# Performance work log

Measured on AMD Instinct MI355X. Metric: run time of the kernel, lower is better.

Reference implementation:

```python
import jax, jax.numpy as jnp
import numpy as np

B, T, W = 64, 64, 20
VIDEO_DIM = 1024
JOINT_DIM = 1024
K, STRIDE = 4, 4
MARGIN = 0.2
EPS = 1e-8


def _l2norm(x, axis=-1):
    n = jnp.sqrt(jnp.sum(x * x, axis=axis, keepdims=True))
    return x / jnp.maximum(n, EPS)


def _conv1d(x, w, b, stride):
    # x: (B, C, L), w: (O, I, K) -> (B, O, L_out), VALID padding (padding=0)
    y = jax.lax.conv_general_dilated(x, w, (stride,), 'VALID',
                                     dimension_numbers=('NCH', 'OIH', 'NCH'))
    return y + b[None, :, None]


def _diag_loss(scores, margin):
    # faithful port of diag(): row/column margin costs with zeroed diagonal
    b = scores.shape[0]
    d = jnp.diagonal(scores)
    off = 1.0 - jnp.eye(b, dtype=scores.dtype)
    cost_s = jnp.maximum(margin + scores - d[:, None], 0.0) * off
    cost_im = jnp.maximum(margin + scores - d[None, :], 0.0) * off
    return cost_s.sum() / b + cost_im.sum() / b


def setup_inputs() -> dict:
    key = jax.random.key(0)
    ks = jax.random.split(key, 10)
    def g(k, shape, scale=0.02):
        return jax.random.normal(k, shape, dtype=jnp.float32) * scale
    return dict(
        video=jax.random.normal(ks[0], (B, T, VIDEO_DIM), dtype=jnp.float32),
        words=jax.random.normal(ks[1], (B, W, JOINT_DIM), dtype=jnp.float32),
        w_masks=jnp.ones((B, W), dtype=jnp.int32),
        sentences=jax.random.normal(ks[2], (B, JOINT_DIM), dtype=jnp.float32),
        conv0_w=g(ks[3], (JOINT_DIM, VIDEO_DIM, K)),
        conv0_b=jnp.zeros((JOINT_DIM,), jnp.float32),
        conv1_w=g(ks[4], (JOINT_DIM, JOINT_DIM, K)),
        conv1_b=jnp.zeros((JOINT_DIM,), jnp.float32),
        conv2_w=g(ks[5], (JOINT_DIM, JOINT_DIM, K)),
        conv2_b=jnp.zeros((JOINT_DIM,), jnp.float32),
        conv1d_w=g(ks[6], (JOINT_DIM, JOINT_DIM, 1)),
        conv1d_b=jnp.zeros((JOINT_DIM,), jnp.float32),
        fc_w=g(ks[7], (JOINT_DIM, JOINT_DIM)),
        fc_b=jnp.zeros((JOINT_DIM,), jnp.float32),
    )


def reference(video, words, w_masks, sentences,
              conv0_w, conv0_b, conv1_w, conv1_b, conv2_w, conv2_b,
              conv1d_w, conv1d_b, fc_w, fc_b):
    # Vectorizes the original per-sample python loop over the pair axes (i=sentence, j=video).
    x = jnp.transpose(video, (0, 2, 1))          # (B, C, T)
    wmask = (w_masks > 0)                        # (B, W)
    conv_params = [(conv0_w, conv0_b), (conv1_w, conv1_b), (conv2_w, conv2_b)]
    sims = []
    v_tmp = x
    for cw, cb in conv_params:
        v_tmp = jax.nn.relu(_conv1d(v_tmp, cw, cb, STRIDE))
        v = jnp.transpose(_conv1d(v_tmp, conv1d_w, conv1d_b, 1), (0, 2, 1))  # (B, Tl, D)
        # frame_by_word: masked softmax attention of frames over words
        att = jnp.einsum('jtd,iwd->ijtw', v, words)            # (i, j, Tl, W)
        att = jnp.where(wmask[:, None, None, :], att, -1e30)
        att = jax.nn.softmax(att, axis=-1)
        v_s = jnp.einsum('ijtw,iwd->ijtd', att, words)         # attended word ctx
        # cosine sim of l2-normed vectors == dot product
        sim = jnp.einsum('jtd,ijtd->ijt', _l2norm(v), _l2norm(v_s))
        sims.append(sim)
    score_all = jnp.concatenate(sims, axis=2)    # (B, B, T_total=21)
    # torch code sorts descending then means over dim 1 -> mean is sort-invariant
    scores = score_all.mean(axis=2)              # (B, B) local scores
    positive_map = score_all[jnp.arange(B), jnp.arange(B)]     # (B, T_total)
    # global branch: final conv output has length 1 -> squeeze
    g_v = _l2norm(v_tmp[:, :, 0] @ fc_w.T + fc_b)              # (B, D), unit norm
    g_scores = _l2norm(sentences) @ g_v.T                      # [i, j] = cos(g_v[j], sent[i])
    loss = _diag_loss(scores, MARGIN) + _diag_loss(g_scores, MARGIN)
    return loss, positive_map
```

## Files before the change

kernel.cpp:

```cpp
#include <hip/hip_runtime.h>
#include <cmath>
#include <cstdint>


typedef __bf16 bf16_t;
typedef bf16_t bf16x8 __attribute__((ext_vector_type(8)));
typedef bf16_t bf16x4 __attribute__((ext_vector_type(4)));
typedef float  f32x4  __attribute__((ext_vector_type(4)));

#define CP0_SL   1048576
#define CP1_SL   262144
#define CPC0_SL  1048576
#define CP2_SL   65536
#define CPC1_SL  262144
#define CPC2_SL  65536
#define CPFC_SL  65536
#define CPAT_SL  1720320

#define MFMA16(a,b,c) __builtin_amdgcn_mfma_f32_16x16x32_bf16(a, b, c, 0, 0, 0)

__device__ __forceinline__ void gload_lds16(const void* g, void* l) {
    __builtin_amdgcn_global_load_lds(
        (const __attribute__((address_space(1))) void*)g,
        (__attribute__((address_space(3))) void*)l, 16, 0, 0);
}

__device__ __forceinline__ int swz(int r, int c) { return (r * 8 + (c ^ (r & 7))) * 8; }

__device__ __forceinline__ void gemm64(
    const bf16_t* __restrict__ A, const bf16_t* __restrict__ B,
    float* __restrict__ Cz, int Nc, int K,
    int m0A, int n0B, int k0, int nIt, int m0C, int n0C,
    bf16_t* sA, bf16_t* sB)
{
    const int tid  = threadIdx.x;
    const int lane = tid & 63, wave = tid >> 6;
    const int sr = tid >> 3, pc = tid & 7, lc = pc ^ (sr & 7);
    const bf16_t* Ag = A + (size_t)(m0A + sr) * K + k0 + lc * 8;
    const bf16_t* Bg = B + (size_t)(n0B + sr) * K + k0 + lc * 8;
    const size_t rowskip = (size_t)32 * K;
    const int wr = (wave >> 1) * 32, wc = (wave & 1) * 32;
    const int fm = lane & 15, cb = lane >> 4;
    int offA[2][2], offB[2][2];
    #pragma unroll
    for (int h = 0; h < 2; h++) {
        offA[h][0] = swz(wr +      fm, cb + h * 4);
        offA[h][1] = swz(wr + 16 + fm, cb + h * 4);
        offB[h][0] = swz(wc +      fm, cb + h * 4);
        offB[h][1] = swz(wc + 16 + fm, cb + h * 4);
    }
    f32x4 acc[2][2];
    #pragma unroll
    for (int a = 0; a < 2; a++)
        #pragma unroll
        for (int b = 0; b < 2; b++) acc[a][b] = (f32x4){0.f, 0.f, 0.f, 0.f};

    gload_lds16(Ag,           sA + tid * 8);
    gload_lds16(Ag + rowskip, sA + 2048 + tid * 8);
    gload_lds16(Bg,           sB + tid * 8);
    gload_lds16(Bg + rowskip, sB + 2048 + tid * 8);
    for (int it = 0; it < nIt; ++it) {
        const int buf = it & 1;
        const bf16_t* cA = sA + buf * 4096;
        const bf16_t* cB = sB + buf * 4096;
        __syncthreads();
        if (it + 1 < nIt) {
            const bf16_t* a = Ag + (it + 1) * 64;
            const bf16_t* b = Bg + (it + 1) * 64;
            bf16_t* dA = sA + (buf ^ 1) * 4096;
            bf16_t* dB = sB + (buf ^ 1) * 4096;
            gload_lds16(a,           dA + tid * 8);
            gload_lds16(a + rowskip, dA + 2048 + tid * 8);
            gload_lds16(b,           dB + tid * 8);
            gload_lds16(b + rowskip, dB + 2048 + tid * 8);
        }
        #pragma unroll
        for (int h = 0; h < 2; h++) {
            bf16x8 a0 = *(const bf16x8*)&cA[offA[h][0]];
            bf16x8 a1 = *(const bf16x8*)&cA[offA[h][1]];
            bf16x8 b0 = *(const bf16x8*)&cB[offB[h][0]];
            bf16x8 b1 = *(const bf16x8*)&cB[offB[h][1]];
            acc[0][0] = MFMA16(a0, b0, acc[0][0]);
            acc[0][1] = MFMA16(a0, b1, acc[0][1]);
            acc[1][0] = MFMA16(a1, b0, acc[1][0]);
            acc[1][1] = MFMA16(a1, b1, acc[1][1]);
        }
    }
    #pragma unroll
    for (int im = 0; im < 2; im++)
        #pragma unroll
        for (int rr = 0; rr < 4; rr++) {
            int gm = m0C + wr + im * 16 + cb * 4 + rr;
            #pragma unroll
            for (int in_ = 0; in_ < 2; in_++) {
                int cg = n0C + wc + in_ * 16 + fm;
                Cz[(size_t)gm * Nc + cg] = acc[im][in_][rr];
            }
        }
}

__device__ __forceinline__ void rownorm_row(const bf16_t* __restrict__ VCb,
                                            float* __restrict__ VN, int r, int tid)
{
    const int lane = tid & 63;
    const bf16_t* x = VCb + ((size_t)r << 10) + lane * 16;
    bf16x8 v0 = *(const bf16x8*)x, v1 = *(const bf16x8*)(x + 8);
    float s = 0.f;
    #pragma unroll
    for (int e = 0; e < 8; e++) {
        float a = (float)v0[e], b = (float)v1[e];
        s += a * a + b * b;
    }
    #pragma unroll
    for (int o = 32; o; o >>= 1) s += __shfl_xor(s, o, 64);
    if (lane == 0) VN[r] = sqrtf(s);
}

__device__ __forceinline__ void sim_compute(
    int i, int c, const float* __restrict__ CPat, const float* __restrict__ VN,
    const float* Gs, const float* msk, float* __restrict__ SA)
{
    float s[20], p[20];
    float mx = -1e30f;
    #pragma unroll
    for (int w = 0; w < 20; w++) {
        size_t q = (size_t)(i * 20 + w) * 1344 + c;
        s[w] = CPat[q] + CPat[q + CPAT_SL];
        if (msk[w] != 0.f) mx = fmaxf(mx, s[w]);
    }
    float denom = 0.f, num = 0.f;
    #pragma unroll
    for (int w = 0; w < 20; w++) {
        p[w] = (msk[w] != 0.f) ? __expf(s[w] - mx) : 0.f;
        denom += p[w];
        num   += p[w] * s[w];
    }
    float quad = 0.f;
    #pragma unroll
    for (int w = 0; w < 20; w++) {
        float cc = 0.f;
        #pragma unroll
        for (int w2 = 0; w2 < 20; w2++) cc += Gs[w * 20 + w2] * p[w2];
        quad += p[w] * cc;
    }
    float dot = num / denom;
    float vsn = sqrtf(fmaxf(quad, 0.f)) / denom;
    float sim = dot / (fmaxf(VN[c], 1e-8f) * fmaxf(vsn, 1e-8f));
    int j, t;
    if (c < 1024)      { j = c >> 4;          t = c & 15; }
    else if (c < 1280) { j = (c - 1024) >> 2; t = 16 + ((c - 1024) & 3); }
    else               { j = c - 1280;        t = 20; }
    SA[((size_t)i * 64 + j) * 21 + t] = sim;
}

__global__ __launch_bounds__(256) void prep0_kernel(
    const float* __restrict__ c0w, bf16_t* __restrict__ WT0,
    const float* __restrict__ video, bf16_t* __restrict__ Vb)
{
    int bx = blockIdx.x;
    if (bx < 4096) {
        int idx = bx * 256 + threadIdx.x;
        int i = idx & 1023, o = idx >> 10;
        float4 v = *(const float4*)(c0w + ((size_t)o << 12) + (i << 2));
        bf16_t* base = WT0 + ((size_t)o << 12) + i;
        base[0]    = (bf16_t)v.x;
        base[1024] = (bf16_t)v.y;
        base[2048] = (bf16_t)v.z;
        base[3072] = (bf16_t)v.w;
    } else {
        int off = ((bx - 4096) * 256 + threadIdx.x) * 4;
        float4 v = *(const float4*)(video + off);
        bf16x4 o4 = { (bf16_t)v.x, (bf16_t)v.y, (bf16_t)v.z, (bf16_t)v.w };
        *(bf16x4*)(Vb + off) = o4;
    }
}

__global__ __launch_bounds__(256) void d2_kernel(
    const bf16_t* __restrict__ Vb, const bf16_t* __restrict__ WT0, float* __restrict__ CP0,
    const float* __restrict__ c1w, const float* __restrict__ c2w,
    bf16_t* __restrict__ WT1, bf16_t* __restrict__ WT2,
    const float* __restrict__ words, bf16_t* __restrict__ Wordsb,
    const float* __restrict__ c1dw, bf16_t* __restrict__ C1b,
    const float* __restrict__ fcw, bf16_t* __restrict__ Fb)
{
    __shared__ __align__(16) bf16_t sA[2][8192];
    __shared__ __align__(16) bf16_t sB[2][8192];
    const int bx = blockIdx.x, tid = threadIdx.x;
    if (bx < 512) {
        const int z = bx >> 6, rem = bx & 63, xt = rem & 7, yt = rem >> 3;
        const int m0 = xt * 128, n0 = yt * 128, k0 = z * 512;
        const int lane = tid & 63, wave = tid >> 6;
        const int sr = tid >> 3, pc = tid & 7, lc = pc ^ (sr & 7);
        const bf16_t* Ag = Vb  + (size_t)(m0 + sr) * 4096 + k0 + lc * 8;
        const bf16_t* Bg = WT0 + (size_t)(n0 + sr) * 4096 + k0 + lc * 8;
        const size_t rowskip = (size_t)32 * 4096;
        const int wrow = (wave >> 1) * 64, wcol = (wave & 1) * 64;
        const int fm = lane & 15, cb = lane >> 4;
        int offA[2][4], offB[2][4];
        #pragma unroll
        for (int h = 0; h < 2; h++)
            #pragma unroll
            for (int m = 0; m < 4; m++) {
                offA[h][m] = swz(wrow + m * 16 + fm, cb + h * 4);
                offB[h][m] = swz(wcol + m * 16 + fm, cb + h * 4);
            }
        f32x4 acc[4][4];
        #pragma unroll
        for (int m = 0; m < 4; m++)
            #pragma unroll
            for (int n = 0; n < 4; n++) acc[m][n] = (f32x4){0.f, 0.f, 0.f, 0.f};

        #pragma unroll
        for (int g = 0; g < 4; g++) {
            gload_lds16(Ag + g * rowskip, &sA[0][tid * 8 + g * 2048]);
            gload_lds16(Bg + g * rowskip, &sB[0][tid * 8 + g * 2048]);
        }
        for (int it = 0; it < 8; ++it) {
            const int buf = it & 1;
            __syncthreads();
            if (it < 7) {
                const bf16_t* a = Ag + (it + 1) * 64;
                const bf16_t* b = Bg + (it + 1) * 64;
                #pragma unroll
                for (int g = 0; g < 4; g++) {
                    gload_lds16(a + g * rowskip, &sA[buf ^ 1][tid * 8 + g * 2048]);
                    gload_lds16(b + g * rowskip, &sB[buf ^ 1][tid * 8 + g * 2048]);
                }
            }
            #pragma unroll
            for (int h = 0; h < 2; h++) {
                bf16x8 av[4], bv[4];
                #pragma unroll
                for (int m = 0; m < 4; m++) {
                    av[m] = *(const bf16x8*)&sA[buf][offA[h][m]];
                    bv[m] = *(const bf16x8*)&sB[buf][offB[h][m]];
                }
                #pragma unroll
                for (int m = 0; m < 4; m++)
                    #pragma unroll
                    for (int n = 0; n < 4; n++)
                        acc[m][n] = MFMA16(av[m], bv[n], acc[m][n]);
            }
        }
        float* Cz = CP0 + (size_t)z * CP0_SL;
        #pragma unroll
        for (int m = 0; m < 4; m++)
            #pragma unroll
            for (int rr = 0; rr < 4; rr++) {
                int gm = m0 + wrow + m * 16 + cb * 4 + rr;
                #pragma unroll
                for (int n = 0; n < 4; n++) {
                    int cg = n0 + wcol + n * 16 + fm;
                    Cz[(size_t)gm * 1024 + cg] = acc[m][n][rr];
                }
            }
    } else if (bx < 8704) {
        const float* w; bf16_t* wt; int b2 = bx - 512;
        if (b2 < 4096) { w = c1w; wt = WT1; }
        else           { w = c2w; wt = WT2; b2 -= 4096; }
        int idx = b2 * 256 + tid;
        int i = idx & 1023, o = idx >> 10;
        float4 v = *(const float4*)(w + ((size_t)o << 12) + (i << 2));
        bf16_t* base = wt + ((size_t)o << 12) + i;
        base[0]    = (bf16_t)v.x;
        base[1024] = (bf16_t)v.y;
        base[2048] = (bf16_t)v.z;
        base[3072] = (bf16_t)v.w;
    } else {
        const float* s; bf16_t* d; int b2 = bx - 8704;
        if (b2 < 1280)      { s = words; d = Wordsb; }
        else if (b2 < 2304) { s = c1dw;  d = C1b; b2 -= 1280; }
        else                { s = fcw;   d = Fb;  b2 -= 2304; }
        int off = (b2 * 256 + tid) * 4;
        float4 v = *(const float4*)(s + off);
        bf16x4 o4 = { (bf16_t)v.x, (bf16_t)v.y, (bf16_t)v.z, (bf16_t)v.w };
        *(bf16x4*)(d + off) = o4;
    }
}

__global__ __launch_bounds__(256) void d3_kernel(
    const float* __restrict__ CP0, const float* __restrict__ c0b,
    bf16_t* __restrict__ Astack, const bf16_t* __restrict__ Wordsb,
    float* __restrict__ GR)
{
    int bx = blockIdx.x;
    if (bx < 4096) {
        int idx = bx * 256 + threadIdx.x;
        int n = idx & 1023;
        float s = c0b[n];
        #pragma unroll
        for (int z = 0; z < 8; z++) s += CP0[(size_t)z * CP0_SL + idx];
        Astack[idx] = (bf16_t)fmaxf(s, 0.f);
    } else {
        int g = bx - 4096;
        int i = g / 100, piece = g % 100;
        int wave = threadIdx.x >> 6, lane = threadIdx.x & 63;
        int pair = piece * 4 + wave;
        int w = pair / 20, w2 = pair % 20;
        const bf16_t* a = Wordsb + (((size_t)i * 20 + w)  << 10) + lane * 16;
        const bf16_t* b = Wordsb + (((size_t)i * 20 + w2) << 10) + lane * 16;
        bf16x8 a0 = *(const bf16x8*)a, a1 = *(const bf16x8*)(a + 8);
        bf16x8 b0 = *(const bf16x8*)b, b1 = *(const bf16x8*)(b + 8);
        float s = 0.f;
        #pragma unroll
        for (int e = 0; e < 8; e++)
            s += (float)a0[e] * (float)b0[e] + (float)a1[e] * (float)b1[e];
        #pragma unroll
        for (int o = 32; o; o >>= 1) s += __shfl_xor(s, o, 64);
        if (lane == 0) GR[(size_t)i * 400 + pair] = s;
    }
}

__global__ __launch_bounds__(256) void d4_kernel(
    const bf16_t* __restrict__ Astack, const bf16_t* __restrict__ WT1,
    const bf16_t* __restrict__ C1b, float* __restrict__ CP1, float* __restrict__ CPc0)
{
    __shared__ __align__(16) bf16_t smem[16384];
    bf16_t* sA = smem; bf16_t* sB = smem + 8192;
    int bx = blockIdx.x;
    if (bx < 512) {
        int z = bx >> 6, rem = bx & 63, xt = rem & 3, yt = rem >> 2;
        gemm64(Astack, WT1, CP1 + (size_t)z * CP1_SL, 1024, 4096,
               xt * 64, yt * 64, z * 512, 8, xt * 64, yt * 64, sA, sB);
    } else {
        int b2 = bx - 512;
        int z = b2 >> 8, rem = b2 & 255, xt = rem & 15, yt = rem >> 4;
        gemm64(Astack, C1b, CPc0 + (size_t)z * CPC0_SL, 1024, 1024,
               xt * 64, yt * 64, z * 512, 8, xt * 64, yt * 64, sA, sB);
    }
}

__global__ __launch_bounds__(256) void d5_kernel(
    const float* __restrict__ CP1, const float* __restrict__ c1b, bf16_t* __restrict__ A2b,
    const float* __restrict__ CPc0, const float* __restrict__ c1db, bf16_t* __restrict__ VCb)
{
    int bx = blockIdx.x;
    if (bx < 1024) {
        int idx = bx * 256 + threadIdx.x;
        int n = idx & 1023;
        float s = c1b[n];
        #pragma unroll
        for (int z = 0; z < 8; z++) s += CP1[(size_t)z * CP1_SL + idx];
        A2b[idx] = (bf16_t)fmaxf(s, 0.f);
    } else {
        int idx = (bx - 1024) * 256 + threadIdx.x;
        int n = idx & 1023;
        float s = CPc0[idx] + CPc0[idx + CPC0_SL] + c1db[n];
        VCb[idx] = (bf16_t)s;
    }
}

__global__ __launch_bounds__(256) void d6_kernel(
    const bf16_t* __restrict__ A2b, const bf16_t* __restrict__ WT2,
    const bf16_t* __restrict__ C1b, const bf16_t* __restrict__ Wordsb,
    const bf16_t* __restrict__ VCb, float* __restrict__ CP2,
    float* __restrict__ CPc1, float* __restrict__ CPat, float* __restrict__ VN)
{
    __shared__ __align__(16) bf16_t smem[16384];
    bf16_t* sA = smem; bf16_t* sB = smem + 8192;
    int bx = blockIdx.x;
    if (bx < 128) {
        int z = bx >> 4, yt = bx & 15;
        gemm64(A2b, WT2, CP2 + (size_t)z * CP2_SL, 1024, 4096,
               0, yt * 64, z * 512, 8, 0, yt * 64, sA, sB);
    } else if (bx < 256) {
        int g = bx - 128;
        int z = g >> 6, rem = g & 63, xt = rem & 3, yt = rem >> 2;
        gemm64(A2b, C1b, CPc1 + (size_t)z * CPC1_SL, 1024, 1024,
               xt * 64, yt * 64, z * 512, 8, xt * 64, yt * 64, sA, sB);
    } else if (bx < 896) {
        int g = bx - 256;
        int z = g / 320, rem = g % 320;
        int xt = rem % 20, yt = rem / 20;
        gemm64(Wordsb, VCb, CPat + (size_t)z * CPAT_SL, 1344, 1024,
               xt * 64, yt * 64, z * 512, 8, xt * 64, yt * 64, sA, sB);
    } else {
        int r = (bx - 896) * 4 + (threadIdx.x >> 6);
        rownorm_row(VCb, VN, r, threadIdx.x);
    }
}

__global__ __launch_bounds__(256) void d7_kernel(
    const float* __restrict__ CP2, const float* __restrict__ c2b,
    const bf16_t* __restrict__ C1b, const bf16_t* __restrict__ Fb,
    float* __restrict__ CPc2, float* __restrict__ CPfc,
    const float* __restrict__ CPc1, const float* __restrict__ c1db,
    bf16_t* __restrict__ VCb, const float* __restrict__ CPat,
    const float* __restrict__ GR, const float* __restrict__ VN,
    const int* __restrict__ wmask, float* __restrict__ SA)
{
    __shared__ __align__(16) bf16_t smem[24576];
    const int bx = blockIdx.x, tid = threadIdx.x;
    if (bx < 128) {
        bf16_t* Abig = smem;
        bf16_t* sB   = smem + 16384;
        const int which = bx >> 6, rem = bx & 63;
        const int z = rem >> 4, yt = rem & 15;
        const int n0 = yt * 64, k0 = z * 256;
        const bf16_t* Bmat = which ? Fb : C1b;
        float* Cz = (which ? CPfc : CPc2) + (size_t)z * 65536;
        #pragma unroll
        for (int qq = 0; qq < 8; qq++) {
            int q = qq * 256 + tid;
            int r = q >> 5, ch = q & 31;
            int col = k0 + ch * 8;
            f32x4 s0 = *(const f32x4*)(c2b + col);
            f32x4 s1 = *(const f32x4*)(c2b + col + 4);
            #pragma unroll
            for (int zz = 0; zz < 8; zz++) {
                const float* p = CP2 + (size_t)zz * CP2_SL + r * 1024 + col;
                s0 += *(const f32x4*)p;
                s1 += *(const f32x4*)(p + 4);
            }
            bf16x8 o;
            #pragma unroll
            for (int e = 0; e < 4; e++) {
                o[e]     = (bf16_t)fmaxf(s0[e], 0.f);
                o[4 + e] = (bf16_t)fmaxf(s1[e], 0.f);
            }
            *(bf16x8*)(Abig + r * 256 + ((ch ^ (r & 7)) << 3)) = o;
        }
        const int lane = tid & 63, wave = tid >> 6;
        const int sr = tid >> 3, pc = tid & 7, lcx = pc ^ (sr & 7);
        const bf16_t* Bg = Bmat + (size_t)(n0 + sr) * 1024 + k0 + lcx * 8;
        const size_t rowskip = (size_t)32 * 1024;
        const int wr = (wave >> 1) * 32, wc = (wave & 1) * 32;
        const int fm = lane & 15, cb = lane >> 4;
        int aoff[2][2], offB[2][2];
        #pragma unroll
        for (int h = 0; h < 2; h++) {
            int r0 = wr + fm, r1 = wr + 16 + fm;
            aoff[h][0] = r0 * 256 + (((cb + 4 * h) ^ (r0 & 7)) << 3);
            aoff[h][1] = r1 * 256 + (((cb + 4 * h) ^ (r1 & 7)) << 3);
            offB[h][0] = swz(wc +      fm, cb + h * 4);
            offB[h][1] = swz(wc + 16 + fm, cb + h * 4);
        }
        f32x4 acc[2][2];
        #pragma unroll
        for (int a = 0; a < 2; a++)
            #pragma unroll
            for (int b = 0; b < 2; b++) acc[a][b] = (f32x4){0.f, 0.f, 0.f, 0.f};
        gload_lds16(Bg,           sB + tid * 8);
        gload_lds16(Bg + rowskip, sB + 2048 + tid * 8);
        for (int it = 0; it < 4; ++it) {
            const int buf = it & 1;
            const bf16_t* cB = sB + buf * 4096;
            __syncthreads();
            if (it < 3) {
                const bf16_t* b = Bg + (it + 1) * 64;
                bf16_t* dB = sB + (buf ^ 1) * 4096;
                gload_lds16(b,           dB + tid * 8);
                gload_lds16(b + rowskip, dB + 2048 + tid * 8);
            }
            #pragma unroll
            for (int h = 0; h < 2; h++) {
                bf16x8 a0 = *(const bf16x8*)&Abig[aoff[h][0] + it * 64];
                bf16x8 a1 = *(const bf16x8*)&Abig[aoff[h][1] + it * 64];
                bf16x8 b0 = *(const bf16x8*)&cB[offB[h][0]];
                bf16x8 b1 = *(const bf16x8*)&cB[offB[h][1]];
                acc[0][0] = MFMA16(a0, b0, acc[0][0]);
                acc[0][1] = MFMA16(a0, b1, acc[0][1]);
                acc[1][0] = MFMA16(a1, b0, acc[1][0]);
                acc[1][1] = MFMA16(a1, b1, acc[1][1]);
            }
        }
        #pragma unroll
        for (int im = 0; im < 2; im++)
            #pragma unroll
            for (int rr = 0; rr < 4; rr++) {
                int gm = wr + im * 16 + cb * 4 + rr;
                #pragma unroll
                for (int in_ = 0; in_ < 2; in_++) {
                    int cg = n0 + wc + in_ * 16 + fm;
                    Cz[(size_t)gm * 1024 + cg] = acc[im][in_][rr];
                }
            }
    } else if (bx < 1152) {
        int idx = (bx - 128) * 256 + tid;
        int n = idx & 1023;
        float s = CPc1[idx] + CPc1[idx + CPC1_SL] + c1db[n];
        VCb[(size_t)(1024 << 10) + idx] = (bf16_t)s;
    } else {
        int s = bx - 1152;
        int i = s >> 2, seg = s & 3;
        float* Gs  = (float*)smem;
        float* msk = Gs + 400;
        for (int q = tid; q < 400; q += 256) Gs[q] = GR[(size_t)i * 400 + q];
        if (tid < 20) msk[tid] = (wmask[i * 20 + tid] != 0) ? 1.f : 0.f;
        __syncthreads();
        sim_compute(i, seg * 256 + tid, CPat, VN, Gs, msk, SA);
    }
}

__global__ __launch_bounds__(256) void d8_kernel(
    const float* __restrict__ CPc2, const float* __restrict__ CPfc,
    const float* __restrict__ c1db, const float* __restrict__ fcb,
    bf16_t* __restrict__ VCb, float* __restrict__ GV,
    const bf16_t* __restrict__ Wordsb, float* __restrict__ CPat,
    float* __restrict__ VN)
{
    __shared__ __align__(16) bf16_t smem[16384];
    bf16_t* sA = smem; bf16_t* sB = smem + 8192;
    int bx = blockIdx.x, tid = threadIdx.x;
    if (bx < 256) {
        int idx = bx * 256 + tid;
        int n = idx & 1023;
        float vc = c1db[n], gv = fcb[n];
        #pragma unroll
        for (int z = 0; z < 4; z++) {
            vc += CPc2[(size_t)z * CPC2_SL + idx];
            gv += CPfc[(size_t)z * CPFC_SL + idx];
        }
        VCb[(size_t)(1280 << 10) + idx] = (bf16_t)vc;
        GV[idx] = gv;
    } else if (bx < 416) {
        int g = bx - 256;
        int z = g / 80, rem = g % 80;
        int xt = rem % 20, yt = rem / 20;
        gemm64(Wordsb, VCb, CPat + (size_t)z * CPAT_SL, 1344, 1024,
               xt * 64, 1024 + yt * 64, z * 512, 8, xt * 64, 1024 + yt * 64, sA, sB);
    } else {
        int r = 1024 + (bx - 416) * 4 + (tid >> 6);
        rownorm_row(VCb, VN, r, tid);
    }
}

__global__ __launch_bounds__(256) void d9_kernel(
    const bf16_t* __restrict__ Wordsb, const bf16_t* __restrict__ VCb,
    float* __restrict__ CPat, float* __restrict__ VN,
    const float* __restrict__ sent, const float* __restrict__ GV,
    float* __restrict__ GS, const float* __restrict__ GR,
    const int* __restrict__ wmask, float* __restrict__ SA)
{
    __shared__ __align__(16) bf16_t smem[16384];
    bf16_t* sA = smem; bf16_t* sB = smem + 8192;
    int bx = blockIdx.x, tid = threadIdx.x;
    if (bx < 40) {
        int z = bx / 20, xt = bx % 20;
        gemm64(Wordsb, VCb, CPat + (size_t)z * CPAT_SL, 1344, 1024,
               xt * 64, 1280, z * 512, 8, xt * 64, 1280, sA, sB);
    } else if (bx < 56) {
        int r = 1280 + (bx - 40) * 4 + (tid >> 6);
        rownorm_row(VCb, VN, r, tid);
    } else if (bx < 1080) {
        int item = (bx - 56) * 4 + (tid >> 6);
        int i = item >> 6, j = item & 63;
        int lane = tid & 63;
        const float* a = sent + (size_t)i * 1024;
        const float* b = GV + (size_t)j * 1024;
        float sab = 0.f, saa = 0.f, sbb = 0.f;
        #pragma unroll
        for (int q = 0; q < 16; q++) {
            int d = lane + 64 * q;
            float av = a[d], bv = b[d];
            sab += av * bv; saa += av * av; sbb += bv * bv;
        }
        #pragma unroll
        for (int o = 32; o; o >>= 1) {
            sab += __shfl_xor(sab, o, 64);
            saa += __shfl_xor(saa, o, 64);
            sbb += __shfl_xor(sbb, o, 64);
        }
        if (lane == 0)
            GS[item] = sab / (fmaxf(sqrtf(saa), 1e-8f) * fmaxf(sqrtf(sbb), 1e-8f));
    } else {
        int i = bx - 1080;
        float* Gs  = (float*)smem;
        float* msk = Gs + 400;
        for (int q = tid; q < 400; q += 256) Gs[q] = GR[(size_t)i * 400 + q];
        if (tid < 20) msk[tid] = (wmask[i * 20 + tid] != 0) ? 1.f : 0.f;
        __syncthreads();
        sim_compute(i, 1024 + tid, CPat, VN, Gs, msk, SA);
    }
}

__global__ __launch_bounds__(256) void d10_kernel(
    const float* __restrict__ CPat, const float* __restrict__ GR,
    const float* __restrict__ VN, const int* __restrict__ wmask,
    float* __restrict__ SA)
{
    __shared__ float Gs[400];
    __shared__ float msk[20];
    int i = blockIdx.x, tid = threadIdx.x;
    for (int q = tid; q < 400; q += 256) Gs[q] = GR[(size_t)i * 400 + q];
    if (tid < 20) msk[tid] = (wmask[i * 20 + tid] != 0) ? 1.f : 0.f;
    __syncthreads();
    if (tid < 64) sim_compute(i, 1280 + tid, CPat, VN, Gs, msk, SA);
}

__global__ __launch_bounds__(256) void d11_kernel(
    const float* __restrict__ SA, float* __restrict__ SC, float* __restrict__ out)
{
    int idx = blockIdx.x * 256 + threadIdx.x;
    int i = idx >> 6, j = idx & 63;
    const float* row = SA + (size_t)idx * 21;
    float s = 0.f;
    #pragma unroll
    for (int t = 0; t < 21; t++) s += row[t];
    SC[idx] = s * (1.0f / 21.0f);
    if (i == j) {
        #pragma unroll
        for (int t = 0; t < 21; t++) out[1 + i * 21 + t] = row[t];
    }
}

__global__ __launch_bounds__(256) void loss_kernel(
    const float* __restrict__ SC_, const float* __restrict__ GS_,
    float* __restrict__ out)
{
    __shared__ float d1[64], d2[64], red[4];
    int tid = threadIdx.x;
    if (tid < 64) { d1[tid] = SC_[tid * 65]; d2[tid] = GS_[tid * 65]; }
    __syncthreads();
    float acc = 0.f;
    for (int idx = tid; idx < 4096; idx += 256) {
        int i = idx >> 6, j = idx & 63;
        if (i != j) {
            float s = SC_[idx];
            acc += fmaxf(0.2f + s - d1[i], 0.f) + fmaxf(0.2f + s - d1[j], 0.f);
            float g = GS_[idx];
            acc += fmaxf(0.2f + g - d2[i], 0.f) + fmaxf(0.2f + g - d2[j], 0.f);
        }
    }
    #pragma unroll
    for (int o = 32; o; o >>= 1) acc += __shfl_xor(acc, o, 64);
    if ((tid & 63) == 0) red[tid >> 6] = acc;
    __syncthreads();
    if (tid == 0) out[0] = (red[0] + red[1] + red[2] + red[3]) * (1.0f / 64.0f);
}

extern "C" void kernel_launch(void* const* d_in, const int* in_sizes, int n_in,
                              void* d_out, int out_size, void* d_ws, size_t ws_size,
                              hipStream_t stream)
{
    const float* video     = (const float*)d_in[0];
    const float* words     = (const float*)d_in[1];
    const int*   w_masks   = (const int*)  d_in[2];
    const float* sentences = (const float*)d_in[3];
    const float* conv0_w   = (const float*)d_in[4];
    const float* conv0_b   = (const float*)d_in[5];
    const float* conv1_w   = (const float*)d_in[6];
    const float* conv1_b   = (const float*)d_in[7];
    const float* conv2_w   = (const float*)d_in[8];
    const float* conv2_b   = (const float*)d_in[9];
    const float* conv1d_w  = (const float*)d_in[10];
    const float* conv1d_b  = (const float*)d_in[11];
    const float* fc_w      = (const float*)d_in[12];
    const float* fc_b      = (const float*)d_in[13];
    float* out = (float*)d_out;
    float* ws = (float*)d_ws;

    bf16_t* WT0    = (bf16_t*)(ws + 0);
    bf16_t* WT1    = (bf16_t*)(ws + 2097152);
    bf16_t* WT2    = (bf16_t*)(ws + 4194304);
    bf16_t* Vb     = (bf16_t*)(ws + 6291456);
    bf16_t* Wordsb = (bf16_t*)(ws + 8388608);
    bf16_t* C1b    = (bf16_t*)(ws + 9043968);
    bf16_t* Fb     = (bf16_t*)(ws + 9568256);
    bf16_t* Astack = (bf16_t*)(ws + 10092544);
    bf16_t* VCb    = (bf16_t*)(ws + 10780672);
    float*  CP0    = ws + 11468800;
    float*  CP1    = ws + 19857408;
    float*  CPc0   = ws + 21954560;
    float*  CP2    = ws + 24051712;
    float*  CPc1   = ws + 24576000;
    float*  CPc2   = ws + 25100288;
    float*  CPfc   = ws + 25362432;
    float*  CPat   = ws + 25624576;
    float*  VN     = ws + 29065216;
    float*  GR     = ws + 29066560;
    float*  SA     = ws + 29092160;
    float*  SC     = ws + 29178176;
    float*  GV     = ws + 29182272;
    float*  GS     = ws + 29247808;

    bf16_t* A2b = Astack + 1048576;

    dim3 blk(256);

    prep0_kernel<<<8192, blk, 0, stream>>>(conv0_w, WT0, video, Vb);
    d2_kernel<<<12032, blk, 0, stream>>>(Vb, WT0, CP0, conv1_w, conv2_w, WT1, WT2,
                                         words, Wordsb, conv1d_w, C1b, fc_w, Fb);
    d3_kernel<<<10496, blk, 0, stream>>>(CP0, conv0_b, Astack, Wordsb, GR);
    d4_kernel<<<1024, blk, 0, stream>>>(Astack, WT1, C1b, CP1, CPc0);
    d5_kernel<<<5120, blk, 0, stream>>>(CP1, conv1_b, A2b, CPc0, conv1d_b, VCb);
    d6_kernel<<<1152, blk, 0, stream>>>(A2b, WT2, C1b, Wordsb, VCb, CP2, CPc1, CPat, VN);
    d7_kernel<<<1408, blk, 0, stream>>>(CP2, conv2_b, C1b, Fb, CPc2, CPfc,
                                        CPc1, conv1d_b, VCb, CPat, GR, VN, w_masks, SA);
    d8_kernel<<<480, blk, 0, stream>>>(CPc2, CPfc, conv1d_b, fc_b, VCb, GV,
                                       Wordsb, CPat, VN);
    d9_kernel<<<1144, blk, 0, stream>>>(Wordsb, VCb, CPat, VN, sentences, GV, GS,
                                        GR, w_masks, SA);
    d10_kernel<<<64, blk, 0, stream>>>(CPat, GR, VN, w_masks, SA);
    d11_kernel<<<16, blk, 0, stream>>>(SA, SC, out);
    loss_kernel<<<1, blk, 0, stream>>>(SC, GS, out);
}
```

Before: 249.7 us.

## Reduce split-K partials, fuse bias epilogues, and coalesce weight transposes via LDS

Removes split-K for the smaller GEMMs: the conv1d, attention and fc GEMMs now run full K in one pass. Their bias-add and bf16 conversion are fused into the GEMM epilogue, which drops the separate reduction passes and one kernel launch. The conv0 GEMM halves its split count from 8 to 4. Weight transposes now go through LDS so the global writes are coalesced, and casts, partial reductions and the word Gram computation are vectorised and staged in LDS. The trade-off is fewer blocks and less parallelism for several GEMMs and longer per-block K loops.

```diff
diff --git a/kernel.cpp b/kernel.cpp
--- a/kernel.cpp
+++ b/kernel.cpp
@@ -6,16 +6,12 @@
 typedef __bf16 bf16_t;
 typedef bf16_t bf16x8 __attribute__((ext_vector_type(8)));
 typedef bf16_t bf16x4 __attribute__((ext_vector_type(4)));
+typedef bf16_t bf16x2 __attribute__((ext_vector_type(2)));
 typedef float  f32x4  __attribute__((ext_vector_type(4)));
 
 #define CP0_SL   1048576
 #define CP1_SL   262144
-#define CPC0_SL  1048576
 #define CP2_SL   65536
-#define CPC1_SL  262144
-#define CPC2_SL  65536
-#define CPFC_SL  65536
-#define CPAT_SL  1720320
 
 #define MFMA16(a,b,c) __builtin_amdgcn_mfma_f32_16x16x32_bf16(a, b, c, 0, 0, 0)
 
@@ -27,11 +23,52 @@
 
 __device__ __forceinline__ int swz(int r, int c) { return (r * 8 + (c ^ (r & 7))) * 8; }
 
+__device__ __forceinline__ void wtrans4(const float* __restrict__ w,
+                                        bf16_t* __restrict__ wt,
+                                        int o0, int tid, bf16_t* lds )
+{
+    #pragma unroll
+    for (int oo = 0; oo < 4; oo++) {
+        const float* src = w + ((size_t)(o0 + oo) << 12);
+        #pragma unroll
+        for (int q = 0; q < 2; q++) {
+            f32x4 va = *(const f32x4*)(src + tid * 16 + q * 8);
+            f32x4 vb = *(const f32x4*)(src + tid * 16 + q * 8 + 4);
+            int ib = tid * 4 + 2 * q;
+            #pragma unroll
+            for (int k = 0; k < 4; k++) {
+                bf16x2 p2 = { (bf16_t)va[k], (bf16_t)vb[k] };
+                *(bf16x2*)(lds + oo * 4096 + k * 1024 + ib) = p2;
+            }
+        }
+    }
+    __syncthreads();
+    #pragma unroll
+    for (int oo = 0; oo < 4; oo++) {
+        bf16x8 v0 = *(bf16x8*)(lds + oo * 4096 + tid * 16);
+        bf16x8 v1 = *(bf16x8*)(lds + oo * 4096 + tid * 16 + 8);
+        bf16_t* dst = wt + ((size_t)(o0 + oo) << 12) + tid * 16;
+        *(bf16x8*)dst       = v0;
+        *(bf16x8*)(dst + 8) = v1;
+    }
+}
+
+__device__ __forceinline__ void cast8(const float* __restrict__ s,
+                                      bf16_t* __restrict__ d, int idx8)
+{
+    f32x4 a = *(const f32x4*)(s + (size_t)idx8 * 8);
+    f32x4 b = *(const f32x4*)(s + (size_t)idx8 * 8 + 4);
+    bf16x8 o;
+    #pragma unroll
+    for (int e = 0; e < 4; e++) { o[e] = (bf16_t)a[e]; o[4 + e] = (bf16_t)b[e]; }
+    *(bf16x8*)(d + (size_t)idx8 * 8) = o;
+}
+
 __device__ __forceinline__ void gemm64(
     const bf16_t* __restrict__ A, const bf16_t* __restrict__ B,
-    float* __restrict__ Cz, int Nc, int K,
-    int m0A, int n0B, int k0, int nIt, int m0C, int n0C,
-    bf16_t* sA, bf16_t* sB)
+    int Nc, int K, int m0A, int n0B, int k0, int nIt, int m0C, int n0C,
+    bf16_t* sA, bf16_t* sB,
+    float* __restrict__ Cf, const float* __restrict__ bias, bf16_t* __restrict__ Dbf)
 {
     const int tid  = threadIdx.x;
     const int lane = tid & 63, wave = tid >> 6;
@@ -94,7 +131,8 @@
             #pragma unroll
             for (int in_ = 0; in_ < 2; in_++) {
                 int cg = n0C + wc + in_ * 16 + fm;
-                Cz[(size_t)gm * Nc + cg] = acc[im][in_][rr];
+                if (Dbf) Dbf[(size_t)gm * Nc + cg] = (bf16_t)(acc[im][in_][rr] + bias[cg]);
+                else     Cf[(size_t)gm * Nc + cg] = acc[im][in_][rr];
             }
         }
 }
@@ -124,8 +162,7 @@
     float mx = -1e30f;
     #pragma unroll
     for (int w = 0; w < 20; w++) {
-        size_t q = (size_t)(i * 20 + w) * 1344 + c;
-        s[w] = CPat[q] + CPat[q + CPAT_SL];
+        s[w] = CPat[(size_t)(i * 20 + w) * 1344 + c];
         if (msk[w] != 0.f) mx = fmaxf(mx, s[w]);
     }
     float denom = 0.f, num = 0.f;
@@ -157,22 +194,10 @@
     const float* __restrict__ c0w, bf16_t* __restrict__ WT0,
     const float* __restrict__ video, bf16_t* __restrict__ Vb)
 {
+    __shared__ __align__(16) bf16_t lds[16384];
     int bx = blockIdx.x;
-    if (bx < 4096) {
-        int idx = bx * 256 + threadIdx.x;
-        int i = idx & 1023, o = idx >> 10;
-        float4 v = *(const float4*)(c0w + ((size_t)o << 12) + (i << 2));
-        bf16_t* base = WT0 + ((size_t)o << 12) + i;
-        base[0]    = (bf16_t)v.x;
-        base[1024] = (bf16_t)v.y;
-        base[2048] = (bf16_t)v.z;
-        base[3072] = (bf16_t)v.w;
-    } else {
-        int off = ((bx - 4096) * 256 + threadIdx.x) * 4;
-        float4 v = *(const float4*)(video + off);
-        bf16x4 o4 = { (bf16_t)v.x, (bf16_t)v.y, (bf16_t)v.z, (bf16_t)v.w };
-        *(bf16x4*)(Vb + off) = o4;
-    }
+    if (bx < 256) wtrans4(c0w, WT0, bx * 4, threadIdx.x, lds);
+    else          cast8(video, Vb, (bx - 256) * 256 + threadIdx.x);
 }
 
 __global__ __launch_bounds__(256) void d2_kernel(
@@ -183,12 +208,13 @@
     const float* __restrict__ c1dw, bf16_t* __restrict__ C1b,
     const float* __restrict__ fcw, bf16_t* __restrict__ Fb)
 {
-    __shared__ __align__(16) bf16_t sA[2][8192];
-    __shared__ __align__(16) bf16_t sB[2][8192];
+    __shared__ __align__(16) bf16_t smem[32768];
     const int bx = blockIdx.x, tid = threadIdx.x;
-    if (bx < 512) {
+    if (bx < 256) {
+        bf16_t* sA = smem;
+        bf16_t* sB = smem + 16384;
         const int z = bx >> 6, rem = bx & 63, xt = rem & 7, yt = rem >> 3;
-        const int m0 = xt * 128, n0 = yt * 128, k0 = z * 512;
+        const int m0 = xt * 128, n0 = yt * 128, k0 = z * 1024;
         const int lane = tid & 63, wave = tid >> 6;
         const int sr = tid >> 3, pc = tid & 7, lc = pc ^ (sr & 7);
         const bf16_t* Ag = Vb  + (size_t)(m0 + sr) * 4096 + k0 + lc * 8;
@@ -212,19 +238,19 @@
 
         #pragma unroll
         for (int g = 0; g < 4; g++) {
-            gload_lds16(Ag + g * rowskip, &sA[0][tid * 8 + g * 2048]);
-            gload_lds16(Bg + g * rowskip, &sB[0][tid * 8 + g * 2048]);
-        }
-        for (int it = 0; it < 8; ++it) {
+            gload_lds16(Ag + g * rowskip, &sA[tid * 8 + g * 2048]);
+            gload_lds16(Bg + g * rowskip, &sB[tid * 8 + g * 2048]);
+        }
+        for (int it = 0; it < 16; ++it) {
             const int buf = it & 1;
             __syncthreads();
-            if (it < 7) {
+            if (it < 15) {
                 const bf16_t* a = Ag + (it + 1) * 64;
                 const bf16_t* b = Bg + (it + 1) * 64;
                 #pragma unroll
                 for (int g = 0; g < 4; g++) {
-                    gload_lds16(a + g * rowskip, &sA[buf ^ 1][tid * 8 + g * 2048]);
-                    gload_lds16(b + g * rowskip, &sB[buf ^ 1][tid * 8 + g * 2048]);
+                    gload_lds16(a + g * rowskip, &sA[(buf ^ 1) * 8192 + tid * 8 + g * 2048]);
+                    gload_lds16(b + g * rowskip, &sB[(buf ^ 1) * 8192 + tid * 8 + g * 2048]);
                 }
             }
             #pragma unroll
@@ -232,8 +258,8 @@
                 bf16x8 av[4], bv[4];
                 #pragma unroll
                 for (int m = 0; m < 4; m++) {
-                    av[m] = *(const bf16x8*)&sA[buf][offA[h][m]];
-                    bv[m] = *(const bf16x8*)&sB[buf][offB[h][m]];
+                    av[m] = *(const bf16x8*)&sA[buf * 8192 + offA[h][m]];
+                    bv[m] = *(const bf16x8*)&sB[buf * 8192 + offB[h][m]];
                 }
                 #pragma unroll
                 for (int m = 0; m < 4; m++)
@@ -254,27 +280,15 @@
                     Cz[(size_t)gm * 1024 + cg] = acc[m][n][rr];
                 }
             }
-    } else if (bx < 8704) {
-        const float* w; bf16_t* wt; int b2 = bx - 512;
-        if (b2 < 4096) { w = c1w; wt = WT1; }
-        else           { w = c2w; wt = WT2; b2 -= 4096; }
-        int idx = b2 * 256 + tid;
-        int i = idx & 1023, o = idx >> 10;
-        float4 v = *(const float4*)(w + ((size_t)o << 12) + (i << 2));
-        bf16_t* base = wt + ((size_t)o << 12) + i;
-        base[0]    = (bf16_t)v.x;
-        base[1024] = (bf16_t)v.y;
-        base[2048] = (bf16_t)v.z;
-        base[3072] = (bf16_t)v.w;
+    } else if (bx < 768) {
+        int b2 = bx - 256;
+        if (b2 < 256) wtrans4(c1w, WT1, b2 * 4, tid, smem);
+        else          wtrans4(c2w, WT2, (b2 - 256) * 4, tid, smem);
     } else {
-        const float* s; bf16_t* d; int b2 = bx - 8704;
-        if (b2 < 1280)      { s = words; d = Wordsb; }
-        else if (b2 < 2304) { s = c1dw;  d = C1b; b2 -= 1280; }
-        else                { s = fcw;   d = Fb;  b2 -= 2304; }
-        int off = (b2 * 256 + tid) * 4;
-        float4 v = *(const float4*)(s + off);
-        bf16x4 o4 = { (bf16_t)v.x, (bf16_t)v.y, (bf16_t)v.z, (bf16_t)v.w };
-        *(bf16x4*)(d + off) = o4;
+        int b2 = bx - 768;
+        if (b2 < 640)       cast8(words, Wordsb, b2 * 256 + tid);
+        else if (b2 < 1152) cast8(c1dw, C1b, (b2 - 640) * 256 + tid);
+        else                cast8(fcw, Fb, (b2 - 1152) * 256 + tid);
     }
 }
 
@@ -283,146 +297,148 @@
     bf16_t* __restrict__ Astack, const bf16_t* __restrict__ Wordsb,
     float* __restrict__ GR)
 {
-    int bx = blockIdx.x;
-    if (bx < 4096) {
-        int idx = bx * 256 + threadIdx.x;
-        int n = idx & 1023;
-        float s = c0b[n];
-        #pragma unroll
-        for (int z = 0; z < 8; z++) s += CP0[(size_t)z * CP0_SL + idx];
-        Astack[idx] = (bf16_t)fmaxf(s, 0.f);
+    __shared__ __align__(16) bf16_t smem[20480];
+    int bx = blockIdx.x, tid = threadIdx.x;
+    if (bx < 512) {
+        int idx8 = bx * 256 + tid;
+        size_t base = (size_t)idx8 * 8;
+        int nb = (int)(base & 1023);
+        f32x4 s0 = *(const f32x4*)(c0b + nb);
+        f32x4 s1 = *(const f32x4*)(c0b + nb + 4);
+        #pragma unroll
+        for (int z = 0; z < 4; z++) {
+            const float* p = CP0 + (size_t)z * CP0_SL + base;
+            s0 += *(const f32x4*)p;
+            s1 += *(const f32x4*)(p + 4);
+        }
+        bf16x8 o;
+        #pragma unroll
+        for (int e = 0; e < 4; e++) {
+            o[e]     = (bf16_t)fmaxf(s0[e], 0.f);
+            o[4 + e] = (bf16_t)fmaxf(s1[e], 0.f);
+        }
+        *(bf16x8*)(Astack + base) = o;
     } else {
-        int g = bx - 4096;
-        int i = g / 100, piece = g % 100;
-        int wave = threadIdx.x >> 6, lane = threadIdx.x & 63;
-        int pair = piece * 4 + wave;
-        int w = pair / 20, w2 = pair % 20;
-        const bf16_t* a = Wordsb + (((size_t)i * 20 + w)  << 10) + lane * 16;
-        const bf16_t* b = Wordsb + (((size_t)i * 20 + w2) << 10) + lane * 16;
-        bf16x8 a0 = *(const bf16x8*)a, a1 = *(const bf16x8*)(a + 8);
-        bf16x8 b0 = *(const bf16x8*)b, b1 = *(const bf16x8*)(b + 8);
-        float s = 0.f;
-        #pragma unroll
-        for (int e = 0; e < 8; e++)
-            s += (float)a0[e] * (float)b0[e] + (float)a1[e] * (float)b1[e];
-        #pragma unroll
-        for (int o = 32; o; o >>= 1) s += __shfl_xor(s, o, 64);
-        if (lane == 0) GR[(size_t)i * 400 + pair] = s;
+        int i = bx - 512;
+        const bf16_t* Wr = Wordsb + (size_t)i * 20480;
+        #pragma unroll
+        for (int c = 0; c < 10; c++)
+            gload_lds16(Wr + (c * 256 + tid) * 8, smem + (c * 256 + tid) * 8);
+        __syncthreads();
+        int wave = tid >> 6, lane = tid & 63;
+        for (int r = 0; r < 100; ++r) {
+            int p = wave * 100 + r;
+            int w1 = p / 20, w2 = p % 20;
+            const bf16_t* a = smem + w1 * 1024 + lane * 16;
+            const bf16_t* b = smem + w2 * 1024 + lane * 16;
+            bf16x8 a0 = *(const bf16x8*)a, a1 = *(const bf16x8*)(a + 8);
+            bf16x8 b0 = *(const bf16x8*)b, b1 = *(const bf16x8*)(b + 8);
+            float s = 0.f;
+            #pragma unroll
+            for (int e = 0; e < 8; e++)
+                s += (float)a0[e] * (float)b0[e] + (float)a1[e] * (float)b1[e];
+            #pragma unroll
+            for (int o = 32; o; o >>= 1) s += __shfl_xor(s, o, 64);
+            if (lane == 0) GR[(size_t)i * 400 + p] = s;
+        }
     }
 }
 
 __global__ __launch_bounds__(256) void d4_kernel(
     const bf16_t* __restrict__ Astack, const bf16_t* __restrict__ WT1,
-    const bf16_t* __restrict__ C1b, float* __restrict__ CP1, float* __restrict__ CPc0)
+    const bf16_t* __restrict__ C1b, const float* __restrict__ c1db,
+    float* __restrict__ CP1, bf16_t* __restrict__ VCb)
 {
     __shared__ __align__(16) bf16_t smem[16384];
     bf16_t* sA = smem; bf16_t* sB = smem + 8192;
     int bx = blockIdx.x;
     if (bx < 512) {
         int z = bx >> 6, rem = bx & 63, xt = rem & 3, yt = rem >> 2;
-        gemm64(Astack, WT1, CP1 + (size_t)z * CP1_SL, 1024, 4096,
-               xt * 64, yt * 64, z * 512, 8, xt * 64, yt * 64, sA, sB);
+        gemm64(Astack, WT1, 1024, 4096, xt * 64, yt * 64, z * 512, 8,
+               xt * 64, yt * 64, sA, sB, CP1 + (size_t)z * CP1_SL, nullptr, nullptr);
     } else {
         int b2 = bx - 512;
-        int z = b2 >> 8, rem = b2 & 255, xt = rem & 15, yt = rem >> 4;
-        gemm64(Astack, C1b, CPc0 + (size_t)z * CPC0_SL, 1024, 1024,
-               xt * 64, yt * 64, z * 512, 8, xt * 64, yt * 64, sA, sB);
+        int xt = b2 & 15, yt = b2 >> 4;
+        gemm64(Astack, C1b, 1024, 1024, xt * 64, yt * 64, 0, 16,
+               xt * 64, yt * 64, sA, sB, nullptr, c1db, VCb);
     }
 }
 
 __global__ __launch_bounds__(256) void d5_kernel(
-    const float* __restrict__ CP1, const float* __restrict__ c1b, bf16_t* __restrict__ A2b,
-    const float* __restrict__ CPc0, const float* __restrict__ c1db, bf16_t* __restrict__ VCb)
-{
-    int bx = blockIdx.x;
-    if (bx < 1024) {
-        int idx = bx * 256 + threadIdx.x;
-        int n = idx & 1023;
-        float s = c1b[n];
-        #pragma unroll
-        for (int z = 0; z < 8; z++) s += CP1[(size_t)z * CP1_SL + idx];
-        A2b[idx] = (bf16_t)fmaxf(s, 0.f);
+    const float* __restrict__ CP1, const float* __restrict__ c1b,
+    bf16_t* __restrict__ A2b, const bf16_t* __restrict__ VCb, float* __restrict__ VN)
+{
+    int bx = blockIdx.x, tid = threadIdx.x;
+    if (bx < 128) {
+        int idx8 = bx * 256 + tid;
+        size_t base = (size_t)idx8 * 8;
+        int nb = (int)(base & 1023);
+        f32x4 s0 = *(const f32x4*)(c1b + nb);
+        f32x4 s1 = *(const f32x4*)(c1b + nb + 4);
+        #pragma unroll
+        for (int z = 0; z < 8; z++) {
+            const float* p = CP1 + (size_t)z * CP1_SL + base;
+            s0 += *(const f32x4*)p;
+            s1 += *(const f32x4*)(p + 4);
+        }
+        bf16x8 o;
+        #pragma unroll
+        for (int e = 0; e < 4; e++) {
+            o[e]     = (bf16_t)fmaxf(s0[e], 0.f);
+            o[4 + e] = (bf16_t)fmaxf(s1[e], 0.f);
+        }
+        *(bf16x8*)(A2b + base) = o;
     } else {
-        int idx = (bx - 1024) * 256 + threadIdx.x;
-        int n = idx & 1023;
-        float s = CPc0[idx] + CPc0[idx + CPC0_SL] + c1db[n];
-        VCb[idx] = (bf16_t)s;
+        int r = (bx - 128) * 4 + (tid >> 6);
+        rownorm_row(VCb, VN, r, tid);
     }
 }
 
 __global__ __launch_bounds__(256) void d6_kernel(
     const bf16_t* __restrict__ A2b, const bf16_t* __restrict__ WT2,
-    const bf16_t* __restrict__ C1b, const bf16_t* __restrict__ Wordsb,
-    const bf16_t* __restrict__ VCb, float* __restrict__ CP2,
-    float* __restrict__ CPc1, float* __restrict__ CPat, float* __restrict__ VN)
+    const bf16_t* __restrict__ C1b, const float* __restrict__ c1db,
+    const bf16_t* __restrict__ Wordsb, bf16_t* __restrict__ VCb,
+    float* __restrict__ CP2, float* __restrict__ CPat)
 {
     __shared__ __align__(16) bf16_t smem[16384];
     bf16_t* sA = smem; bf16_t* sB = smem + 8192;
     int bx = blockIdx.x;
     if (bx < 128) {
         int z = bx >> 4, yt = bx & 15;
-        gemm64(A2b, WT2, CP2 + (size_t)z * CP2_SL, 1024, 4096,
-               0, yt * 64, z * 512, 8, 0, yt * 64, sA, sB);
-    } else if (bx < 256) {
+        gemm64(A2b, WT2, 1024, 4096, 0, yt * 64, z * 512, 8,
+               0, yt * 64, sA, sB, CP2 + (size_t)z * CP2_SL, nullptr, nullptr);
+    } else if (bx < 192) {
         int g = bx - 128;
-        int z = g >> 6, rem = g & 63, xt = rem & 3, yt = rem >> 2;
-        gemm64(A2b, C1b, CPc1 + (size_t)z * CPC1_SL, 1024, 1024,
-               xt * 64, yt * 64, z * 512, 8, xt * 64, yt * 64, sA, sB);
-    } else if (bx < 896) {
-        int g = bx - 256;
-        int z = g / 320, rem = g % 320;
-        int xt = rem % 20, yt = rem / 20;
-        gemm64(Wordsb, VCb, CPat + (size_t)z * CPAT_SL, 1344, 1024,
-               xt * 64, yt * 64, z * 512, 8, xt * 64, yt * 64, sA, sB);
+        int xt = g & 3, yt = g >> 2;
+        gemm64(A2b, C1b, 1024, 1024, xt * 64, yt * 64, 0, 16,
+               1024 + xt * 64, yt * 64, sA, sB, nullptr, c1db, VCb);
     } else {
-        int r = (bx - 896) * 4 + (threadIdx.x >> 6);
-        rownorm_row(VCb, VN, r, threadIdx.x);
+        int g = bx - 192;
+        int xt = g % 20, yt = g / 20;
+        gemm64(Wordsb, VCb, 1344, 1024, xt * 64, yt * 64, 0, 16,
+               xt * 64, yt * 64, sA, sB, CPat, nullptr, nullptr);
     }
 }
 
 __global__ __launch_bounds__(256) void d7_kernel(
     const float* __restrict__ CP2, const float* __restrict__ c2b,
     const bf16_t* __restrict__ C1b, const bf16_t* __restrict__ Fb,
-    float* __restrict__ CPc2, float* __restrict__ CPfc,
-    const float* __restrict__ CPc1, const float* __restrict__ c1db,
-    bf16_t* __restrict__ VCb, const float* __restrict__ CPat,
-    const float* __restrict__ GR, const float* __restrict__ VN,
+    const float* __restrict__ c1db, const float* __restrict__ fcb,
+    bf16_t* __restrict__ VCb, float* __restrict__ GV,
+    const bf16_t* __restrict__ Wordsb, float* __restrict__ CPat,
+    const float* __restrict__ GR, float* __restrict__ VN,
     const int* __restrict__ wmask, float* __restrict__ SA)
 {
     __shared__ __align__(16) bf16_t smem[24576];
     const int bx = blockIdx.x, tid = threadIdx.x;
-    if (bx < 128) {
+    if (bx < 32) {
         bf16_t* Abig = smem;
         bf16_t* sB   = smem + 16384;
-        const int which = bx >> 6, rem = bx & 63;
-        const int z = rem >> 4, yt = rem & 15;
-        const int n0 = yt * 64, k0 = z * 256;
+        const int which = bx >> 4, yt = bx & 15;
+        const int n0 = yt * 64;
         const bf16_t* Bmat = which ? Fb : C1b;
-        float* Cz = (which ? CPfc : CPc2) + (size_t)z * 65536;
-        #pragma unroll
-        for (int qq = 0; qq < 8; qq++) {
-            int q = qq * 256 + tid;
-            int r = q >> 5, ch = q & 31;
-            int col = k0 + ch * 8;
-            f32x4 s0 = *(const f32x4*)(c2b + col);
-            f32x4 s1 = *(const f32x4*)(c2b + col + 4);
-            #pragma unroll
-            for (int zz = 0; zz < 8; zz++) {
-                const float* p = CP2 + (size_t)zz * CP2_SL + r * 1024 + col;
-                s0 += *(const f32x4*)p;
-                s1 += *(const f32x4*)(p + 4);
-            }
-            bf16x8 o;
-            #pragma unroll
-            for (int e = 0; e < 4; e++) {
-                o[e]     = (bf16_t)fmaxf(s0[e], 0.f);
-                o[4 + e] = (bf16_t)fmaxf(s1[e], 0.f);
-            }
-            *(bf16x8*)(Abig + r * 256 + ((ch ^ (r & 7)) << 3)) = o;
-        }
         const int lane = tid & 63, wave = tid >> 6;
         const int sr = tid >> 3, pc = tid & 7, lcx = pc ^ (sr & 7);
-        const bf16_t* Bg = Bmat + (size_t)(n0 + sr) * 1024 + k0 + lcx * 8;
         const size_t rowskip = (size_t)32 * 1024;
         const int wr = (wave >> 1) * 32, wc = (wave & 1) * 32;
         const int fm = lane & 15, cb = lane >> 4;
@@ -440,28 +456,55 @@
         for (int a = 0; a < 2; a++)
             #pragma unroll
             for (int b = 0; b < 2; b++) acc[a][b] = (f32x4){0.f, 0.f, 0.f, 0.f};
-        gload_lds16(Bg,           sB + tid * 8);
-        gload_lds16(Bg + rowskip, sB + 2048 + tid * 8);
-        for (int it = 0; it < 4; ++it) {
-            const int buf = it & 1;
-            const bf16_t* cB = sB + buf * 4096;
+
+        for (int zc = 0; zc < 4; zc++) {
+            const int k0 = zc * 256;
             __syncthreads();
-            if (it < 3) {
-                const bf16_t* b = Bg + (it + 1) * 64;
-                bf16_t* dB = sB + (buf ^ 1) * 4096;
-                gload_lds16(b,           dB + tid * 8);
-                gload_lds16(b + rowskip, dB + 2048 + tid * 8);
-            }
-            #pragma unroll
-            for (int h = 0; h < 2; h++) {
-                bf16x8 a0 = *(const bf16x8*)&Abig[aoff[h][0] + it * 64];
-                bf16x8 a1 = *(const bf16x8*)&Abig[aoff[h][1] + it * 64];
-                bf16x8 b0 = *(const bf16x8*)&cB[offB[h][0]];
-                bf16x8 b1 = *(const bf16x8*)&cB[offB[h][1]];
-                acc[0][0] = MFMA16(a0, b0, acc[0][0]);
-                acc[0][1] = MFMA16(a0, b1, acc[0][1]);
-                acc[1][0] = MFMA16(a1, b0, acc[1][0]);
-                acc[1][1] = MFMA16(a1, b1, acc[1][1]);
+            #pragma unroll
+            for (int qq = 0; qq < 8; qq++) {
+                int q = qq * 256 + tid;
+                int r = q >> 5, ch = q & 31;
+                int col = k0 + ch * 8;
+                f32x4 s0 = *(const f32x4*)(c2b + col);
+                f32x4 s1 = *(const f32x4*)(c2b + col + 4);
+                #pragma unroll
+                for (int zz = 0; zz < 8; zz++) {
+                    const float* p = CP2 + (size_t)zz * CP2_SL + r * 1024 + col;
+                    s0 += *(const f32x4*)p;
+                    s1 += *(const f32x4*)(p + 4);
+                }
+                bf16x8 o;
+                #pragma unroll
+                for (int e = 0; e < 4; e++) {
+                    o[e]     = (bf16_t)fmaxf(s0[e], 0.f);
+                    o[4 + e] = (bf16_t)fmaxf(s1[e], 0.f);
+                }
+                *(bf16x8*)(Abig + r * 256 + ((ch ^ (r & 7)) << 3)) = o;
+            }
+            const bf16_t* Bg = Bmat + (size_t)(n0 + sr) * 1024 + k0 + lcx * 8;
+            gload_lds16(Bg,           sB + tid * 8);
+            gload_lds16(Bg + rowskip, sB + 2048 + tid * 8);
+            for (int it = 0; it < 4; ++it) {
+                const int buf = it & 1;
+                const bf16_t* cB = sB + buf * 4096;
+                __syncthreads();
+                if (it < 3) {
+                    const bf16_t* b = Bg + (it + 1) * 64;
+                    bf16_t* dB = sB + (buf ^ 1) * 4096;
+                    gload_lds16(b,           dB + tid * 8);
+                    gload_lds16(b + rowskip, dB + 2048 + tid * 8);
+                }
+                #pragma unroll
+                for (int h = 0; h < 2; h++) {
+                    bf16x8 a0 = *(const bf16x8*)&Abig[aoff[h][0] + it * 64];
+                    bf16x8 a1 = *(const bf16x8*)&Abig[aoff[h][1] + it * 64];
+                    bf16x8 b0 = *(const bf16x8*)&cB[offB[h][0]];
+                    bf16x8 b1 = *(const bf16x8*)&cB[offB[h][1]];
+                    acc[0][0] = MFMA16(a0, b0, acc[0][0]);
+                    acc[0][1] = MFMA16(a0, b1, acc[0][1]);
+                    acc[1][0] = MFMA16(a1, b0, acc[1][0]);
+                    acc[1][1] = MFMA16(a1, b1, acc[1][1]);
+                }
             }
         }
         #pragma unroll
@@ -472,16 +515,13 @@
                 #pragma unroll
                 for (int in_ = 0; in_ < 2; in_++) {
                     int cg = n0 + wc + in_ * 16 + fm;
-                    Cz[(size_t)gm * 1024 + cg] = acc[im][in_][rr];
+                    float v = acc[im][in_][rr];
+                    if (which) GV[(size_t)gm * 1024 + cg] = v + fcb[cg];
+                    else VCb[(size_t)(1280 + gm) * 1024 + cg] = (bf16_t)(v + c1db[cg]);
                 }
             }
-    } else if (bx < 1152) {
-        int idx = (bx - 128) * 256 + tid;
-        int n = idx & 1023;
-        float s = CPc1[idx] + CPc1[idx + CPC1_SL] + c1db[n];
-        VCb[(size_t)(1024 << 10) + idx] = (bf16_t)s;
-    } else {
-        int s = bx - 1152;
+    } else if (bx < 288) {
+        int s = bx - 32;
         int i = s >> 2, seg = s & 3;
         float* Gs  = (float*)smem;
         float* msk = Gs + 400;
@@ -489,43 +529,19 @@
         if (tid < 20) msk[tid] = (wmask[i * 20 + tid] != 0) ? 1.f : 0.f;
         __syncthreads();
         sim_compute(i, seg * 256 + tid, CPat, VN, Gs, msk, SA);
+    } else if (bx < 352) {
+        int r = 1024 + (bx - 288) * 4 + (tid >> 6);
+        rownorm_row(VCb, VN, r, tid);
+    } else {
+        int g = bx - 352;
+        int xt = g % 20, yt = g / 20;
+        bf16_t* sA = smem; bf16_t* sB = smem + 8192;
+        gemm64(Wordsb, VCb, 1344, 1024, xt * 64, 1024 + yt * 64, 0, 16,
+               xt * 64, 1024 + yt * 64, sA, sB, CPat, nullptr, nullptr);
     }
 }
 
 __global__ __launch_bounds__(256) void d8_kernel(
-    const float* __restrict__ CPc2, const float* __restrict__ CPfc,
-    const float* __restrict__ c1db, const float* __restrict__ fcb,
-    bf16_t* __restrict__ VCb, float* __restrict__ GV,
-    const bf16_t* __restrict__ Wordsb, float* __restrict__ CPat,
-    float* __restrict__ VN)
-{
-    __shared__ __align__(16) bf16_t smem[16384];
-    bf16_t* sA = smem; bf16_t* sB = smem + 8192;
-    int bx = blockIdx.x, tid = threadIdx.x;
-    if (bx < 256) {
-        int idx = bx * 256 + tid;
-        int n = idx & 1023;
-        float vc = c1db[n], gv = fcb[n];
-        #pragma unroll
-        for (int z = 0; z < 4; z++) {
-            vc += CPc2[(size_t)z * CPC2_SL + idx];
-            gv += CPfc[(size_t)z * CPFC_SL + idx];
-        }
-        VCb[(size_t)(1280 << 10) + idx] = (bf16_t)vc;
-        GV[idx] = gv;
-    } else if (bx < 416) {
-        int g = bx - 256;
-        int z = g / 80, rem = g % 80;
-        int xt = rem % 20, yt = rem / 20;
-        gemm64(Wordsb, VCb, CPat + (size_t)z * CPAT_SL, 1344, 1024,
-               xt * 64, 1024 + yt * 64, z * 512, 8, xt * 64, 1024 + yt * 64, sA, sB);
-    } else {
-        int r = 1024 + (bx - 416) * 4 + (tid >> 6);
-        rownorm_row(VCb, VN, r, tid);
-    }
-}
-
-__global__ __launch_bounds__(256) void d9_kernel(
     const bf16_t* __restrict__ Wordsb, const bf16_t* __restrict__ VCb,
     float* __restrict__ CPat, float* __restrict__ VN,
     const float* __restrict__ sent, const float* __restrict__ GV,
@@ -535,15 +551,14 @@
     __shared__ __align__(16) bf16_t smem[16384];
     bf16_t* sA = smem; bf16_t* sB = smem + 8192;
     int bx = blockIdx.x, tid = threadIdx.x;
-    if (bx < 40) {
-        int z = bx / 20, xt = bx % 20;
-        gemm64(Wordsb, VCb, CPat + (size_t)z * CPAT_SL, 1344, 1024,
-               xt * 64, 1280, z * 512, 8, xt * 64, 1280, sA, sB);
-    } else if (bx < 56) {
-        int r = 1280 + (bx - 40) * 4 + (tid >> 6);
+    if (bx < 20) {
+        gemm64(Wordsb, VCb, 1344, 1024, bx * 64, 1280, 0, 16,
+               bx * 64, 1280, sA, sB, CPat, nullptr, nullptr);
+    } else if (bx < 36) {
+        int r = 1280 + (bx - 20) * 4 + (tid >> 6);
         rownorm_row(VCb, VN, r, tid);
-    } else if (bx < 1080) {
-        int item = (bx - 56) * 4 + (tid >> 6);
+    } else if (bx < 1060) {
+        int item = (bx - 36) * 4 + (tid >> 6);
         int i = item >> 6, j = item & 63;
         int lane = tid & 63;
         const float* a = sent + (size_t)i * 1024;
@@ -564,7 +579,7 @@
         if (lane == 0)
             GS[item] = sab / (fmaxf(sqrtf(saa), 1e-8f) * fmaxf(sqrtf(sbb), 1e-8f));
     } else {
-        int i = bx - 1080;
+        int i = bx - 1060;
         float* Gs  = (float*)smem;
         float* msk = Gs + 400;
         for (int q = tid; q < 400; q += 256) Gs[q] = GR[(size_t)i * 400 + q];
@@ -574,7 +589,7 @@
     }
 }
 
-__global__ __launch_bounds__(256) void d10_kernel(
+__global__ __launch_bounds__(256) void d9_kernel(
     const float* __restrict__ CPat, const float* __restrict__ GR,
     const float* __restrict__ VN, const int* __restrict__ wmask,
     float* __restrict__ SA)
@@ -588,7 +603,7 @@
     if (tid < 64) sim_compute(i, 1280 + tid, CPat, VN, Gs, msk, SA);
 }
 
-__global__ __launch_bounds__(256) void d11_kernel(
+__global__ __launch_bounds__(256) void d10_kernel(
     const float* __restrict__ SA, float* __restrict__ SC, float* __restrict__ out)
 {
     int idx = blockIdx.x * 256 + threadIdx.x;
@@ -658,40 +673,33 @@
     bf16_t* C1b    = (bf16_t*)(ws + 9043968);
     bf16_t* Fb     = (bf16_t*)(ws + 9568256);
     bf16_t* Astack = (bf16_t*)(ws + 10092544);
-    bf16_t* VCb    = (bf16_t*)(ws + 10780672);
-    float*  CP0    = ws + 11468800;
-    float*  CP1    = ws + 19857408;
-    float*  CPc0   = ws + 21954560;
-    float*  CP2    = ws + 24051712;
-    float*  CPc1   = ws + 24576000;
-    float*  CPc2   = ws + 25100288;
-    float*  CPfc   = ws + 25362432;
-    float*  CPat   = ws + 25624576;
-    float*  VN     = ws + 29065216;
-    float*  GR     = ws + 29066560;
-    float*  SA     = ws + 29092160;
-    float*  SC     = ws + 29178176;
-    float*  GV     = ws + 29182272;
-    float*  GS     = ws + 29247808;
-
-    bf16_t* A2b = Astack + 1048576;
+    bf16_t* A2b    = (bf16_t*)(ws + 10616832);
+    bf16_t* VCb    = (bf16_t*)(ws + 10747904);
+    float*  CP0    = ws + 11436032;
+    float*  CP1    = ws + 15630336;
+    float*  CP2    = ws + 17727488;
+    float*  CPat   = ws + 18251776;
+    float*  VN     = ws + 19972096;
+    float*  GR     = ws + 19973440;
+    float*  SA     = ws + 19999040;
+    float*  SC     = ws + 20085056;
+    float*  GV     = ws + 20089152;
+    float*  GS     = ws + 20154688;
 
     dim3 blk(256);
 
-    prep0_kernel<<<8192, blk, 0, stream>>>(conv0_w, WT0, video, Vb);
-    d2_kernel<<<12032, blk, 0, stream>>>(Vb, WT0, CP0, conv1_w, conv2_w, WT1, WT2,
-                                         words, Wordsb, conv1d_w, C1b, fc_w, Fb);
-    d3_kernel<<<10496, blk, 0, stream>>>(CP0, conv0_b, Astack, Wordsb, GR);
-    d4_kernel<<<1024, blk, 0, stream>>>(Astack, WT1, C1b, CP1, CPc0);
-    d5_kernel<<<5120, blk, 0, stream>>>(CP1, conv1_b, A2b, CPc0, conv1d_b, VCb);
-    d6_kernel<<<1152, blk, 0, stream>>>(A2b, WT2, C1b, Wordsb, VCb, CP2, CPc1, CPat, VN);
-    d7_kernel<<<1408, blk, 0, stream>>>(CP2, conv2_b, C1b, Fb, CPc2, CPfc,
-                                        CPc1, conv1d_b, VCb, CPat, GR, VN, w_masks, SA);
-    d8_kernel<<<480, blk, 0, stream>>>(CPc2, CPfc, conv1d_b, fc_b, VCb, GV,
-                                       Wordsb, CPat, VN);
-    d9_kernel<<<1144, blk, 0, stream>>>(Wordsb, VCb, CPat, VN, sentences, GV, GS,
+    prep0_kernel<<<2304, blk, 0, stream>>>(conv0_w, WT0, video, Vb);
+    d2_kernel<<<2432, blk, 0, stream>>>(Vb, WT0, CP0, conv1_w, conv2_w, WT1, WT2,
+                                        words, Wordsb, conv1d_w, C1b, fc_w, Fb);
+    d3_kernel<<<576, blk, 0, stream>>>(CP0, conv0_b, Astack, Wordsb, GR);
+    d4_kernel<<<768, blk, 0, stream>>>(Astack, WT1, C1b, conv1d_b, CP1, VCb);
+    d5_kernel<<<384, blk, 0, stream>>>(CP1, conv1_b, A2b, VCb, VN);
+    d6_kernel<<<512, blk, 0, stream>>>(A2b, WT2, C1b, conv1d_b, Wordsb, VCb, CP2, CPat);
+    d7_kernel<<<432, blk, 0, stream>>>(CP2, conv2_b, C1b, Fb, conv1d_b, fc_b,
+                                       VCb, GV, Wordsb, CPat, GR, VN, w_masks, SA);
+    d8_kernel<<<1124, blk, 0, stream>>>(Wordsb, VCb, CPat, VN, sentences, GV, GS,
                                         GR, w_masks, SA);
-    d10_kernel<<<64, blk, 0, stream>>>(CPat, GR, VN, w_masks, SA);
-    d11_kernel<<<16, blk, 0, stream>>>(SA, SC, out);
+    d9_kernel<<<64, blk, 0, stream>>>(CPat, GR, VN, w_masks, SA);
+    d10_kernel<<<16, blk, 0, stream>>>(SA, SC, out);
     loss_kernel<<<1, blk, 0, stream>>>(SC, GS, out);
 }
```

Result: slower. 329.9 us (+32.1%).
